# Kernel tuning notes

Measured on AMD Instinct MI355X. Metric: run time of the kernel, lower is better.

The kernel has to match this reference:

```python
import jax, jax.numpy as jnp
import numpy as np

N_VERT = 20000


def _gather_pad(feat, adj):
    # feat: [B, N, C]; adj: [B, N, K] with 1-based indices, 0 = padding (-> zeros)
    B, N, C = feat.shape
    padded = jnp.concatenate([jnp.zeros((B, 1, C), feat.dtype), feat], axis=1)  # [B, N+1, C]
    return jax.vmap(lambda p, a: p[a])(padded, adj)  # [B, N, K, C]


def setup_inputs() -> dict:
    key = jax.random.key(0)
    ks = jax.random.split(key, 7)
    B, N, K, M, C, O = 4, N_VERT, 16, 9, 64, 64
    x = jax.random.normal(ks[0], (B, N, C), jnp.float32)
    adj = jax.random.randint(ks[1], (B, N, K), 0, N + 1, jnp.int32)  # 0 == no neighbor
    W = jax.random.normal(ks[2], (M, O, C), jnp.float32) * 0.1
    b = jax.random.normal(ks[3], (O,), jnp.float32) * 0.1
    u = jax.random.normal(ks[4], (M, C), jnp.float32) * 0.1
    v = jax.random.normal(ks[5], (M, C), jnp.float32) * 0.1
    c = jax.random.normal(ks[6], (M,), jnp.float32) * 0.1
    return {"x": x, "adj": adj, "W": W, "b": b, "u": u, "v": v, "c": c}


def reference(x, adj, W, b, u, v, c):
    # FEAST graph conv, non-invariant path.
    mask = adj != 0  # [B, N, K]
    # attention logits: u.x_i + v.x_j + c, masked (padding) neighbors -> 0 + c
    ux = jnp.einsum('bnc,mc->bnm', x, u)          # [B, N, M]
    vx = jnp.einsum('bnc,mc->bnm', x, v)          # [B, N, M]
    vxn = _gather_pad(vx, adj)                    # [B, N, K, M]
    logits = jnp.where(mask[..., None], ux[:, :, None, :] + vxn, 0.0) + c
    q = jax.nn.softmax(logits, axis=-1)           # softmax over M kernels
    # gather raw neighbor features (zero for padding), contract q over K first,
    # then apply per-kernel W (linear, so order is equivalent to original wx-gather)
    xn = _gather_pad(x, adj)                      # [B, N, K, C]
    s = jnp.einsum('bnkm,bnkc->bnmc', q, xn)      # [B, N, M, C]
    out = jnp.einsum('bnmc,moc->bno', s, W)       # [B, N, O]
    deg = jnp.sum(mask, axis=-1).astype(x.dtype)  # [B, N]
    inv_deg = jnp.where(deg > 0, 1.0 / jnp.maximum(deg, 1.0), 0.0)
    return out * inv_deg[..., None] + b
```

## Files before the change

kernel.cpp:

```cpp
#include <hip/hip_runtime.h>
#include <cstdint>
#include <cstddef>

#define BB 4
#define NN 20000
#define KK 16
#define MM 9
#define CC 64
#define OO 64
#define BN (BB*NN)
#define MC (MM*CC)
#define UVP 12
#define QNP 272
#define SCP 72
#define SNP (MM*SCP)
#define NKS (MC/32)

typedef _Float16 f16x8 __attribute__((ext_vector_type(8)));
typedef _Float16 f16x4 __attribute__((ext_vector_type(4)));
typedef __fp16   fp16v2 __attribute__((ext_vector_type(2)));
typedef float    f32x4 __attribute__((ext_vector_type(4)));
typedef unsigned short u16;
typedef unsigned int   u32;

union Hcv { _Float16 h; u16 u; };
__device__ __forceinline__ u16 f2h(float f) { Hcv t; t.h = (_Float16)f; return t.u; }
__device__ __forceinline__ float h2f(u16 h) { Hcv t; t.u = h; return (float)t.h; }

__global__ __launch_bounds__(256) void setup_kernel(
    const float* __restrict__ x, const float* __restrict__ W,
    const float* __restrict__ u, const float* __restrict__ v,
    u16* __restrict__ xh, u16* __restrict__ xl,
    u16* __restrict__ wfb2, u16* __restrict__ Gh, u16* __restrict__ Gl)
{
    int bid = blockIdx.x;
    if (bid < 5000) {
        int i = bid * 1024 + threadIdx.x * 4;
        float4 xv = *(const float4*)(x + i);
        u16 h0 = f2h(xv.x), h1 = f2h(xv.y), h2 = f2h(xv.z), h3 = f2h(xv.w);
        ushort4 hv; hv.x = h0; hv.y = h1; hv.z = h2; hv.w = h3;
        *(ushort4*)(xh + i) = hv;
        ushort4 lv;
        lv.x = f2h(xv.x - h2f(h0)); lv.y = f2h(xv.y - h2f(h1));
        lv.z = f2h(xv.z - h2f(h2)); lv.w = f2h(xv.w - h2f(h3));
        *(ushort4*)(xl + i) = lv;
    } else if (bid < 5144) {
        int i = (bid - 5000) * 256 + threadIdx.x;
        int j = i & 7, o = (i >> 3) & 63, lhi = (i >> 9) & 3, ks = i >> 11;
        int kf = ks * 32 + lhi * 8 + j;
        int m = kf >> 6, cc = kf & 63;
        wfb2[i] = f2h(W[m * 4096 + o * 64 + cc]);
    } else {
        int i = (bid - 5144) * 256 + threadIdx.x;
        int r = i >> 6, cc = i & 63;
        float val = (r < 9) ? u[r * 64 + cc] : ((r < 18) ? v[(r - 9) * 64 + cc] : 0.f);
        u16 h = f2h(val);
        Gh[i] = h;
        Gl[i] = f2h(val - h2f(h));
    }
}

__global__ __launch_bounds__(256) void uxvx_kernel(
    const u16* __restrict__ xh, const u16* __restrict__ xl,
    const u16* __restrict__ Gh, const u16* __restrict__ Gl,
    const float* __restrict__ c, float* __restrict__ uxc, float* __restrict__ vxp)
{
    const int wave = threadIdx.x >> 6, lane = threadIdx.x & 63;
    const int lr = lane & 15, lhi = lane >> 4;
    const int t0 = blockIdx.x * 64 + wave * 16;

    const u16* xrh = xh + (size_t)(t0 + lr) * 64 + lhi * 8;
    const u16* xrl = xl + (size_t)(t0 + lr) * 64 + lhi * 8;
    f16x8 ah0 = *(const f16x8*)(xrh), ah1 = *(const f16x8*)(xrh + 32);
    f16x8 al0 = *(const f16x8*)(xrl), al1 = *(const f16x8*)(xrl + 32);

    f32x4 acc0 = {0.f,0.f,0.f,0.f}, acc1 = {0.f,0.f,0.f,0.f};
    #pragma unroll
    for (int t = 0; t < 2; ++t) {
        f32x4 acc = {0.f,0.f,0.f,0.f};
        #pragma unroll
        for (int s = 0; s < 2; ++s) {
            f16x8 gh = *(const f16x8*)(Gh + (t * 16 + lr) * 64 + s * 32 + lhi * 8);
            f16x8 gl = *(const f16x8*)(Gl + (t * 16 + lr) * 64 + s * 32 + lhi * 8);
            f16x8 as  = s ? ah1 : ah0;
            f16x8 asl = s ? al1 : al0;
            acc = __builtin_amdgcn_mfma_f32_16x16x32_f16(as,  gh, acc, 0, 0, 0);
            acc = __builtin_amdgcn_mfma_f32_16x16x32_f16(as,  gl, acc, 0, 0, 0);
            acc = __builtin_amdgcn_mfma_f32_16x16x32_f16(asl, gh, acc, 0, 0, 0);
        }
        if (t == 0) acc0 = acc; else acc1 = acc;
    }

    float cv = (lr < 9) ? c[lr] : 0.f;
    #pragma unroll
    for (int reg = 0; reg < 4; ++reg) {
        int node = t0 + lhi * 4 + reg;
        if (lr < 9) uxc[(size_t)node * UVP + lr] = acc0[reg] + cv;
        else        vxp[(size_t)node * UVP + (lr - 9)] = acc0[reg];
        if (lr < 2) vxp[(size_t)node * UVP + 7 + lr] = acc1[reg];
    }
}

__global__ __launch_bounds__(256) void fused_kernel(
    const u16* __restrict__ xh, const int* __restrict__ adj,
    const float* __restrict__ uxc, const float* __restrict__ vxp,
    const u16* __restrict__ wfb2, const float* __restrict__ bias,
    float* __restrict__ out)
{
    __shared__ __align__(16) u16 qlds[16 * QNP];
    __shared__ __align__(16) u16 slds[16 * SNP];
    const int tid = threadIdx.x, wave = tid >> 6, lane = tid & 63;
    const int lr = lane & 15, lhi = lane >> 4;
    const int node0 = blockIdx.x * 16;
    const int b = node0 / NN;
    const int rowbase = b * NN;

    const int g = lhi;
    const int k = lr;
    const int node = node0 + wave * 4 + g;
    int jj = adj[(size_t)node0 * KK + tid];
    unsigned long long bal = __ballot(jj != 0);
    int deg = __popcll((bal >> (g * 16)) & 0xffffull);
    float inv = (deg > 0) ? (1.0f / (float)deg) : 0.0f;

    float q[MM];
    #pragma unroll
    for (int m = 0; m < MM; ++m) q[m] = 0.f;
    if (jj != 0) {
        const float4* ur = (const float4*)(uxc + (size_t)node * UVP);
        const float4* vr = (const float4*)(vxp + ((size_t)rowbase + (jj - 1)) * UVP);
        float4 u0 = ur[0], u1 = ur[1], u2 = ur[2];
        float4 v0 = vr[0], v1 = vr[1], v2 = vr[2];
        float l[MM] = { u0.x+v0.x, u0.y+v0.y, u0.z+v0.z, u0.w+v0.w,
                        u1.x+v1.x, u1.y+v1.y, u1.z+v1.z, u1.w+v1.w,
                        u2.x+v2.x };
        float mx = l[0];
        #pragma unroll
        for (int m = 1; m < MM; ++m) mx = fmaxf(mx, l[m]);
        float sum = 0.f;
        #pragma unroll
        for (int m = 0; m < MM; ++m) { l[m] = __expf(l[m] - mx); sum += l[m]; }
        float sc = inv / sum;
        #pragma unroll
        for (int m = 0; m < MM; ++m) q[m] = l[m] * sc;
    }
    {
        u16* qw = qlds + (wave * 4 + g) * QNP + k;
        #pragma unroll
        for (int m = 0; m < MM; ++m) qw[m * 16] = f2h(q[m]);
    }

    f16x8 idf[2];
    #pragma unroll
    for (int s = 0; s < 2; ++s) {
        union { u16 us[8]; f16x8 v; } t;
        #pragma unroll
        for (int j = 0; j < 8; ++j)
            t.us[j] = (lhi * 8 + j == s * 16 + lr) ? (u16)0x3C00 : (u16)0;
        idf[s] = t.v;
    }

    const u16* xhb = xh + ((size_t)rowbase << 6);
    #pragma unroll 1
    for (int g2 = 0; g2 < 4; ++g2) {
        const int rnode = wave * 4 + g2;
        int e = __builtin_amdgcn_ds_bpermute((g2 * 16 + lr) * 4, jj);
        int erow = ((e > 0) ? e : 1) - 1;
        const u16* rp = xhb + ((size_t)erow << 6) + lhi * 8;
        f16x8 aLo = *(const f16x8*)(rp);
        f16x8 aHi = *(const f16x8*)(rp + 32);
        f16x4 qf = *(const f16x4*)(qlds + rnode * QNP + lr * 16 + lhi * 4);

        #pragma unroll
        for (int cc = 0; cc < 4; ++cc) {
            f32x4 xt = {0.f,0.f,0.f,0.f};
            xt = __builtin_amdgcn_mfma_f32_16x16x32_f16(
                     (cc < 2) ? aLo : aHi, idf[cc & 1], xt, 0, 0, 0);
            union { fp16v2 h2[2]; f16x4 h4; } at;
            at.h2[0] = __builtin_amdgcn_cvt_pkrtz(xt[0], xt[1]);
            at.h2[1] = __builtin_amdgcn_cvt_pkrtz(xt[2], xt[3]);
            f32x4 d2 = {0.f,0.f,0.f,0.f};
            d2 = __builtin_amdgcn_mfma_f32_16x16x16f16(at.h4, qf, d2, 0, 0, 0);
            if (lr < 9) {
                u32 lo = __builtin_amdgcn_perm((u32)f2h(d2[1]), (u32)f2h(d2[0]), 0x05040100u);
                u32 hi = __builtin_amdgcn_perm((u32)f2h(d2[3]), (u32)f2h(d2[2]), 0x05040100u);
                uint2* p = (uint2*)(slds + rnode * SNP + lr * SCP + cc * 16 + lhi * 4);
                *p = make_uint2(lo, hi);
            }
        }
    }
    __syncthreads();

    const int o0 = wave * 16;
    f32x4 acc = {0.f,0.f,0.f,0.f};
    #pragma unroll
    for (int ks = 0; ks < NKS; ++ks) {
        int kf = ks * 32 + lhi * 8;
        int m = kf >> 6, coff = kf & 63;
        f16x8 afrag = *(const f16x8*)(slds + lr * SNP + m * SCP + coff);
        f16x8 bfrag = *(const f16x8*)(wfb2 + (size_t)(((ks * 4 + lhi) * 64) + o0 + lr) * 8);
        acc = __builtin_amdgcn_mfma_f32_16x16x32_f16(afrag, bfrag, acc, 0, 0, 0);
    }
    float bv = bias[o0 + lr];
    #pragma unroll
    for (int reg = 0; reg < 4; ++reg) {
        int rr = node0 + lhi * 4 + reg;
        out[(size_t)rr * OO + o0 + lr] = acc[reg] + bv;
    }
}

extern "C" void kernel_launch(void* const* d_in, const int* in_sizes, int n_in,
                              void* d_out, int out_size, void* d_ws, size_t ws_size,
                              hipStream_t stream)
{
    const float* x   = (const float*)d_in[0];
    const int*   adj = (const int*)  d_in[1];
    const float* W   = (const float*)d_in[2];
    const float* b   = (const float*)d_in[3];
    const float* u   = (const float*)d_in[4];
    const float* v   = (const float*)d_in[5];
    const float* c   = (const float*)d_in[6];
    float* out = (float*)d_out;

    float* uxc = (float*)d_ws;
    float* vxp = uxc + (size_t)BN * UVP;
    u16*   xh  = (u16*)(vxp + (size_t)BN * UVP);
    u16*   xl  = xh + (size_t)BN * CC;
    u16*   wfb2= xl + (size_t)BN * CC;
    u16*   Gh  = wfb2 + (size_t)NKS * 2048;
    u16*   Gl  = Gh + 2048;

    setup_kernel<<<5152, 256, 0, stream>>>(x, W, u, v, xh, xl, wfb2, Gh, Gl);
    uxvx_kernel<<<1250, 256, 0, stream>>>(xh, xl, Gh, Gl, c, uxc, vxp);
    fused_kernel<<<5000, 256, 0, stream>>>(xh, adj, uxc, vxp, wfb2, b, out);
}
```

Before: 140.6 us.

## Drop xl buffer, split x in uxvx kernel, prefetch gathers, swizzle LDS

The setup kernel no longer writes the low-part fp16 copy of x. The uxvx kernel now reads fp32 x directly and splits it into hi/lo halves in registers, which removes a full-size global write and read. In the fused kernel, all four neighbor-row gathers and q fragments are loaded up front before the MFMA loop, and the loop is fully unrolled so load latency overlaps compute. The q LDS stride shrinks and the s LDS writes and reads use an XOR swizzle to reduce bank conflicts, at the cost of higher register pressure.

```diff
diff --git a/kernel.cpp b/kernel.cpp
--- a/kernel.cpp
+++ b/kernel.cpp
@@ -11,7 +11,7 @@
 #define BN (BB*NN)
 #define MC (MM*CC)
 #define UVP 12
-#define QNP 272
+#define QNP 160
 #define SCP 72
 #define SNP (MM*SCP)
 #define NKS (MC/32)
@@ -30,20 +30,16 @@
 __global__ __launch_bounds__(256) void setup_kernel(
     const float* __restrict__ x, const float* __restrict__ W,
     const float* __restrict__ u, const float* __restrict__ v,
-    u16* __restrict__ xh, u16* __restrict__ xl,
-    u16* __restrict__ wfb2, u16* __restrict__ Gh, u16* __restrict__ Gl)
+    u16* __restrict__ xh, u16* __restrict__ wfb2,
+    u16* __restrict__ Gh, u16* __restrict__ Gl)
 {
     int bid = blockIdx.x;
     if (bid < 5000) {
         int i = bid * 1024 + threadIdx.x * 4;
         float4 xv = *(const float4*)(x + i);
-        u16 h0 = f2h(xv.x), h1 = f2h(xv.y), h2 = f2h(xv.z), h3 = f2h(xv.w);
-        ushort4 hv; hv.x = h0; hv.y = h1; hv.z = h2; hv.w = h3;
+        ushort4 hv;
+        hv.x = f2h(xv.x); hv.y = f2h(xv.y); hv.z = f2h(xv.z); hv.w = f2h(xv.w);
         *(ushort4*)(xh + i) = hv;
-        ushort4 lv;
-        lv.x = f2h(xv.x - h2f(h0)); lv.y = f2h(xv.y - h2f(h1));
-        lv.z = f2h(xv.z - h2f(h2)); lv.w = f2h(xv.w - h2f(h3));
-        *(ushort4*)(xl + i) = lv;
     } else if (bid < 5144) {
         int i = (bid - 5000) * 256 + threadIdx.x;
         int j = i & 7, o = (i >> 3) & 63, lhi = (i >> 9) & 3, ks = i >> 11;
@@ -61,7 +57,7 @@
 }
 
 __global__ __launch_bounds__(256) void uxvx_kernel(
-    const u16* __restrict__ xh, const u16* __restrict__ xl,
+    const float* __restrict__ x,
     const u16* __restrict__ Gh, const u16* __restrict__ Gl,
     const float* __restrict__ c, float* __restrict__ uxc, float* __restrict__ vxp)
 {
@@ -69,10 +65,18 @@
     const int lr = lane & 15, lhi = lane >> 4;
     const int t0 = blockIdx.x * 64 + wave * 16;
 
-    const u16* xrh = xh + (size_t)(t0 + lr) * 64 + lhi * 8;
-    const u16* xrl = xl + (size_t)(t0 + lr) * 64 + lhi * 8;
-    f16x8 ah0 = *(const f16x8*)(xrh), ah1 = *(const f16x8*)(xrh + 32);
-    f16x8 al0 = *(const f16x8*)(xrl), al1 = *(const f16x8*)(xrl + 32);
+    const float* xr = x + (size_t)(t0 + lr) * 64 + lhi * 8;
+    float xf[16];
+    *(float4*)(xf + 0)  = *(const float4*)(xr + 0);
+    *(float4*)(xf + 4)  = *(const float4*)(xr + 4);
+    *(float4*)(xf + 8)  = *(const float4*)(xr + 32);
+    *(float4*)(xf + 12) = *(const float4*)(xr + 36);
+    union { u16 us[8]; f16x8 v; } H0, L0, H1, L1;
+    #pragma unroll
+    for (int i = 0; i < 8; ++i) {
+        u16 h = f2h(xf[i]);      H0.us[i] = h; L0.us[i] = f2h(xf[i] - h2f(h));
+        u16 h2 = f2h(xf[8 + i]); H1.us[i] = h2; L1.us[i] = f2h(xf[8 + i] - h2f(h2));
+    }
 
     f32x4 acc0 = {0.f,0.f,0.f,0.f}, acc1 = {0.f,0.f,0.f,0.f};
     #pragma unroll
@@ -82,8 +86,8 @@
         for (int s = 0; s < 2; ++s) {
             f16x8 gh = *(const f16x8*)(Gh + (t * 16 + lr) * 64 + s * 32 + lhi * 8);
             f16x8 gl = *(const f16x8*)(Gl + (t * 16 + lr) * 64 + s * 32 + lhi * 8);
-            f16x8 as  = s ? ah1 : ah0;
-            f16x8 asl = s ? al1 : al0;
+            f16x8 as  = s ? H1.v : H0.v;
+            f16x8 asl = s ? L1.v : L0.v;
             acc = __builtin_amdgcn_mfma_f32_16x16x32_f16(as,  gh, acc, 0, 0, 0);
             acc = __builtin_amdgcn_mfma_f32_16x16x32_f16(as,  gl, acc, 0, 0, 0);
             acc = __builtin_amdgcn_mfma_f32_16x16x32_f16(asl, gh, acc, 0, 0, 0);
@@ -107,7 +111,7 @@
     const u16* __restrict__ wfb2, const float* __restrict__ bias,
     float* __restrict__ out)
 {
-    __shared__ __align__(16) u16 qlds[16 * QNP];
+    __shared__ __align__(16) u16 qlds[16 * QNP + 96];
     __shared__ __align__(16) u16 slds[16 * SNP];
     const int tid = threadIdx.x, wave = tid >> 6, lane = tid & 63;
     const int lr = lane & 15, lhi = lane >> 4;
@@ -161,30 +165,37 @@
     }
 
     const u16* xhb = xh + ((size_t)rowbase << 6);
-    #pragma unroll 1
+    f16x8 aLo[4], aHi[4];
+    f16x4 qf[4];
+    #pragma unroll
     for (int g2 = 0; g2 < 4; ++g2) {
-        const int rnode = wave * 4 + g2;
         int e = __builtin_amdgcn_ds_bpermute((g2 * 16 + lr) * 4, jj);
         int erow = ((e > 0) ? e : 1) - 1;
         const u16* rp = xhb + ((size_t)erow << 6) + lhi * 8;
-        f16x8 aLo = *(const f16x8*)(rp);
-        f16x8 aHi = *(const f16x8*)(rp + 32);
-        f16x4 qf = *(const f16x4*)(qlds + rnode * QNP + lr * 16 + lhi * 4);
-
+        aLo[g2] = *(const f16x8*)(rp);
+        aHi[g2] = *(const f16x8*)(rp + 32);
+        qf[g2]  = *(const f16x4*)(qlds + (wave * 4 + g2) * QNP + lr * 16 + lhi * 4);
+    }
+
+    #pragma unroll
+    for (int g2 = 0; g2 < 4; ++g2) {
+        const int rnode = wave * 4 + g2;
+        const int swz = ((rnode >> 3) & 1) * 32;
         #pragma unroll
         for (int cc = 0; cc < 4; ++cc) {
             f32x4 xt = {0.f,0.f,0.f,0.f};
             xt = __builtin_amdgcn_mfma_f32_16x16x32_f16(
-                     (cc < 2) ? aLo : aHi, idf[cc & 1], xt, 0, 0, 0);
+                     (cc < 2) ? aLo[g2] : aHi[g2], idf[cc & 1], xt, 0, 0, 0);
             union { fp16v2 h2[2]; f16x4 h4; } at;
             at.h2[0] = __builtin_amdgcn_cvt_pkrtz(xt[0], xt[1]);
             at.h2[1] = __builtin_amdgcn_cvt_pkrtz(xt[2], xt[3]);
             f32x4 d2 = {0.f,0.f,0.f,0.f};
-            d2 = __builtin_amdgcn_mfma_f32_16x16x16f16(at.h4, qf, d2, 0, 0, 0);
+            d2 = __builtin_amdgcn_mfma_f32_16x16x16f16(at.h4, qf[g2], d2, 0, 0, 0);
             if (lr < 9) {
                 u32 lo = __builtin_amdgcn_perm((u32)f2h(d2[1]), (u32)f2h(d2[0]), 0x05040100u);
                 u32 hi = __builtin_amdgcn_perm((u32)f2h(d2[3]), (u32)f2h(d2[2]), 0x05040100u);
-                uint2* p = (uint2*)(slds + rnode * SNP + lr * SCP + cc * 16 + lhi * 4);
+                uint2* p = (uint2*)(slds + rnode * SNP + lr * SCP
+                                    + ((cc * 16 + lhi * 4) ^ swz));
                 *p = make_uint2(lo, hi);
             }
         }
@@ -192,12 +203,13 @@
     __syncthreads();
 
     const int o0 = wave * 16;
+    const int swzR = ((lr >> 3) & 1) * 32;
     f32x4 acc = {0.f,0.f,0.f,0.f};
     #pragma unroll
     for (int ks = 0; ks < NKS; ++ks) {
         int kf = ks * 32 + lhi * 8;
         int m = kf >> 6, coff = kf & 63;
-        f16x8 afrag = *(const f16x8*)(slds + lr * SNP + m * SCP + coff);
+        f16x8 afrag = *(const f16x8*)(slds + lr * SNP + m * SCP + (coff ^ swzR));
         f16x8 bfrag = *(const f16x8*)(wfb2 + (size_t)(((ks * 4 + lhi) * 64) + o0 + lr) * 8);
         acc = __builtin_amdgcn_mfma_f32_16x16x32_f16(afrag, bfrag, acc, 0, 0, 0);
     }
@@ -225,12 +237,11 @@
     float* uxc = (float*)d_ws;
     float* vxp = uxc + (size_t)BN * UVP;
     u16*   xh  = (u16*)(vxp + (size_t)BN * UVP);
-    u16*   xl  = xh + (size_t)BN * CC;
-    u16*   wfb2= xl + (size_t)BN * CC;
+    u16*   wfb2= xh + (size_t)BN * CC;
     u16*   Gh  = wfb2 + (size_t)NKS * 2048;
     u16*   Gl  = Gh + 2048;
 
-    setup_kernel<<<5152, 256, 0, stream>>>(x, W, u, v, xh, xl, wfb2, Gh, Gl);
-    uxvx_kernel<<<1250, 256, 0, stream>>>(xh, xl, Gh, Gl, c, uxc, vxp);
+    setup_kernel<<<5152, 256, 0, stream>>>(x, W, u, v, xh, wfb2, Gh, Gl);
+    uxvx_kernel<<<1250, 256, 0, stream>>>(x, Gh, Gl, c, uxc, vxp);
     fused_kernel<<<5000, 256, 0, stream>>>(xh, adj, uxc, vxp, wfb2, b, out);
 }
```

After: 139.0 us. About the same (-1.1%).
